# Kernel optimization log

Measured on AMD Instinct MI355X. Metric: run time of the kernel, lower is better.

Reference implementation:

```python
import jax, jax.numpy as jnp
import numpy as np

N_NODES = 100000
N_EDGES = 600000
DIMS = [128, 64, 32, 2]


def gcn_conv(x, edge_index, W, b, n_nodes):
    """PyG GCNConv (eval mode): symmetric-normalized aggregation with self-loops.
    out = D^{-1/2} (A + I) D^{-1/2} (x W) + b
    """
    h = x @ W  # [N, out] -- transform first (cheaper when out < in)
    src = jnp.concatenate([edge_index[0], jnp.arange(n_nodes)])  # add self-loops
    dst = jnp.concatenate([edge_index[1], jnp.arange(n_nodes)])
    deg = jax.ops.segment_sum(jnp.ones_like(dst, dtype=h.dtype), dst,
                              num_segments=n_nodes)  # in-degree incl. self-loop
    dinv = jax.lax.rsqrt(deg)
    norm = dinv[src] * dinv[dst]  # [E+N]
    msg = norm[:, None] * h[src]  # gather + scale
    out = jax.ops.segment_sum(msg, dst, num_segments=n_nodes)  # scatter-add
    return out + b


def setup_inputs() -> dict:
    key = jax.random.key(0)
    ks = jax.random.split(key, 8)
    x = jax.random.normal(ks[0], (N_NODES, DIMS[0]), dtype=jnp.float32)
    edge_index = jax.random.randint(ks[1], (2, N_EDGES), 0, N_NODES, dtype=jnp.int64)
    inp = {"x": x, "edge_index": edge_index}
    for i in range(3):
        fan_in, fan_out = DIMS[i], DIMS[i + 1]
        s = 1.0 / np.sqrt(fan_in)
        inp[f"W{i+1}"] = jax.random.uniform(ks[2 + 2 * i], (fan_in, fan_out),
                                            minval=-s, maxval=s, dtype=jnp.float32)
        inp[f"b{i+1}"] = jnp.zeros((fan_out,), dtype=jnp.float32)
    return inp


def reference(x, edge_index, W1, b1, W2, b2, W3, b3):
    # 3 stacked GCNConv layers with ReLU; dropout is identity in eval mode.
    n = x.shape[0]
    x = jax.nn.relu(gcn_conv(x, edge_index, W1, b1, n))
    x = jax.nn.relu(gcn_conv(x, edge_index, W2, b2, n))
    x = jax.nn.relu(gcn_conv(x, edge_index, W3, b3, n))
    return x
```

## Files before the change

kernel.cpp:

```cpp
#include <hip/hip_runtime.h>
#include <math.h>


#define FULL_GRID 2048
#define PARTS 8

typedef const __attribute__((address_space(1))) void* gas_ptr;
typedef __attribute__((address_space(3))) void* las_ptr;
typedef __attribute__((ext_vector_type(8))) short bf16x8;
typedef __attribute__((ext_vector_type(4))) float f32x4;

__device__ __forceinline__ void gld16(const void* g, void* l) {
  __builtin_amdgcn_global_load_lds((gas_ptr)g, (las_ptr)l, 16, 0, 0);
}

__device__ __forceinline__ unsigned short f2bf(float f) {
  unsigned int u = __float_as_uint(f);
  u += 0x7FFF + ((u >> 16) & 1);
  return (unsigned short)(u >> 16);
}
__device__ __forceinline__ float bf2f(unsigned short h) {
  return __uint_as_float(((unsigned int)h) << 16);
}

__global__ __launch_bounds__(256) void k_init(int* __restrict__ p, int n4,
                                              const unsigned int* __restrict__ words,
                                              int* __restrict__ flag,
                                              const float* __restrict__ W1,
                                              const float* __restrict__ W2,
                                              short* __restrict__ Wh1,
                                              short* __restrict__ Wl1,
                                              short* __restrict__ Wh2,
                                              short* __restrict__ Wl2) {
  if (blockIdx.x == 128) {
    __shared__ int sm[256];
    int cnt = 0;
    #pragma unroll
    for (int j = 0; j < 8; ++j) {
      int idx = (threadIdx.x * 8 + j) * 2 + 1;
      cnt += (words[idx] == 0u) ? 1 : 0;
    }
    sm[threadIdx.x] = cnt;
    __syncthreads();
    for (int off = 128; off > 0; off >>= 1) {
      if (threadIdx.x < off) sm[threadIdx.x] += sm[threadIdx.x + off];
      __syncthreads();
    }
    if (threadIdx.x == 0) flag[0] = (sm[0] > 1024) ? 1 : 0;
    return;
  }
  if (blockIdx.x > 128) {
    const int t = (blockIdx.x - 129) * 256 + threadIdx.x;
    const int stride = 32 * 256;
    for (int q = t; q < 4 * 4 * 64 * 8; q += stride) {
      const int e = q & 7, lane = (q >> 3) & 63, nt = (q >> 9) & 3, kt = q >> 11;
      const int k = kt * 32 + (lane >> 4) * 8 + e;
      const int nn = nt * 16 + (lane & 15);
      const float f = W1[k * 64 + nn];
      const unsigned short h = f2bf(f);
      Wh1[q] = (short)h;
      Wl1[q] = (short)f2bf(f - bf2f(h));
    }
    for (int q = t; q < 2 * 2 * 64 * 8; q += stride) {
      const int e = q & 7, lane = (q >> 3) & 63, nt = (q >> 9) & 1, kt = q >> 10;
      const int k = kt * 32 + (lane >> 4) * 8 + e;
      const int nn = nt * 16 + (lane & 15);
      const float f = W2[k * 32 + nn];
      const unsigned short h = f2bf(f);
      Wh2[q] = (short)h;
      Wl2[q] = (short)f2bf(f - bf2f(h));
    }
    return;
  }
  int i = blockIdx.x * blockDim.x + threadIdx.x;
  const int stride = 128 * blockDim.x;
  int4* p4 = (int4*)p;
  for (; i < n4; i += stride) p4[i] = make_int4(0, 0, 0, 0);
}

__global__ __launch_bounds__(256) void k_normalize(const void* __restrict__ eraw,
                                                   int E,
                                                   const int* __restrict__ flag,
                                                   int* __restrict__ srcn,
                                                   int* __restrict__ dstn) {
  const int is64 = flag[0];
  int i = blockIdx.x * blockDim.x + threadIdx.x;
  const int stride = gridDim.x * blockDim.x;
  if (is64) {
    const long long* e = (const long long*)eraw;
    for (; i < E; i += stride) {
      srcn[i] = (int)e[i];
      dstn[i] = (int)e[(long long)E + i];
    }
  } else {
    const int* e = (const int*)eraw;
    for (; i < E; i += stride) {
      srcn[i] = e[i];
      dstn[i] = e[E + i];
    }
  }
}

__global__ __launch_bounds__(256) void k_hist(const int* __restrict__ dstn, int E,
                                              int N, int* __restrict__ counts) {
  const int part = blockIdx.x & (PARTS - 1);
  const int lo = (int)((long long)N * part / PARTS);
  const int hi = (int)((long long)N * (part + 1) / PARTS);
  int i = (blockIdx.x >> 3) * blockDim.x + threadIdx.x;
  const int stride = (gridDim.x >> 3) * blockDim.x;
  for (; i < E; i += stride) {
    const int d = dstn[i];
    if (d >= lo && d < hi) atomicAdd(&counts[d], 1);
  }
}

__global__ __launch_bounds__(1024) void k_scan1(const int* __restrict__ counts,
                                                int* __restrict__ scanned,
                                                int* __restrict__ partials, int n) {
  __shared__ int sm[1024];
  const int i = blockIdx.x * 1024 + threadIdx.x;
  const int v = (i < n) ? counts[i] : 0;
  sm[threadIdx.x] = v;
  __syncthreads();
  for (int off = 1; off < 1024; off <<= 1) {
    int t = sm[threadIdx.x];
    int u = (threadIdx.x >= off) ? sm[threadIdx.x - off] : 0;
    __syncthreads();
    sm[threadIdx.x] = t + u;
    __syncthreads();
  }
  const int inc = sm[threadIdx.x];
  if (i < n) scanned[i] = inc - v;
  if (threadIdx.x == 1023) partials[blockIdx.x] = inc;
}

__global__ __launch_bounds__(256) void k_scan3(const int* __restrict__ scanned,
                                               const int* __restrict__ partials,
                                               int nb,
                                               const int* __restrict__ counts,
                                               int* __restrict__ offsets,
                                               int* __restrict__ cursor,
                                               float* __restrict__ dinv, int n) {
  __shared__ int ps[1024];
  for (int t = threadIdx.x; t < nb; t += 256) ps[t] = partials[t];
  __syncthreads();
  if (threadIdx.x == 0) {
    int run = 0;
    for (int b = 0; b < nb; ++b) { const int v = ps[b]; ps[b] = run; run += v; }
  }
  __syncthreads();
  int i = blockIdx.x * blockDim.x + threadIdx.x;
  const int stride = gridDim.x * blockDim.x;
  for (; i < n; i += stride) {
    const int o = scanned[i] + ps[i >> 10];
    offsets[i] = o;
    cursor[i] = o;
    dinv[i] = rsqrtf((float)counts[i] + 1.0f);
  }
}

__global__ __launch_bounds__(256) void k_fill(const int* __restrict__ srcn,
                                              const int* __restrict__ dstn, int E,
                                              int N, int* __restrict__ cursor,
                                              int* __restrict__ elist) {
  const int part = blockIdx.x & (PARTS - 1);
  const int lo = (int)((long long)N * part / PARTS);
  const int hi = (int)((long long)N * (part + 1) / PARTS);
  int i = (blockIdx.x >> 3) * blockDim.x + threadIdx.x;
  const int stride = (gridDim.x >> 3) * blockDim.x;
  for (; i < E; i += stride) {
    const int d = dstn[i];
    if (d >= lo && d < hi) elist[atomicAdd(&cursor[d], 1)] = srcn[i];
  }
}

template <int F_IN, int F_OUT>
__global__ __launch_bounds__(256) void k_transform_mfma(
    const float* __restrict__ X, const short* __restrict__ Wh,
    const short* __restrict__ Wl, const float* __restrict__ dinv,
    float* __restrict__ H, int n) {
  constexpr int KT = F_IN / 32;
  constexpr int NT = F_OUT / 16;
  constexpr int K4f = F_IN / 4;
  constexpr int SLOTS = F_IN / 8;
  constexpr int TILE_M = 64;
  constexpr int WFRAG = KT * NT * 64 * 8;
  static_assert((WFRAG * 2) % 1024 == 0, "W segs");

  __shared__ __align__(16) unsigned short Xh[TILE_M * F_IN];
  __shared__ __align__(16) unsigned short Xl[TILE_M * F_IN];
  __shared__ __align__(16) unsigned short Whs[WFRAG];
  __shared__ __align__(16) unsigned short Wls[WFRAG];

  const int tid = threadIdx.x;
  const int lane = tid & 63;
  const int wid = tid >> 6;
  const long long base = (long long)blockIdx.x * TILE_M;

  constexpr int WSEGS = WFRAG * 2 / 1024;
  for (int seg = wid; seg < WSEGS; seg += 4) {
    gld16((const char*)Wh + seg * 1024 + lane * 16, (char*)Whs + seg * 1024);
    gld16((const char*)Wl + seg * 1024 + lane * 16, (char*)Wls + seg * 1024);
  }

  const float4* __restrict__ X4 = (const float4*)X;
  for (int g = tid; g < TILE_M * K4f; g += 256) {
    const int row = g / K4f, c4 = g % K4f;
    float4 v = make_float4(0.f, 0.f, 0.f, 0.f);
    if (base + row < n) v = X4[(base + row) * K4f + c4];
    ushort4 hv, lv;
    hv.x = f2bf(v.x); lv.x = f2bf(v.x - bf2f(hv.x));
    hv.y = f2bf(v.y); lv.y = f2bf(v.y - bf2f(hv.y));
    hv.z = f2bf(v.z); lv.z = f2bf(v.z - bf2f(hv.z));
    hv.w = f2bf(v.w); lv.w = f2bf(v.w - bf2f(hv.w));
    const int slot = (c4 >> 1) ^ (row & (SLOTS - 1));
    const int boff = row * (F_IN * 2) + slot * 16 + (c4 & 1) * 8;
    *(ushort4*)((char*)Xh + boff) = hv;
    *(ushort4*)((char*)Xl + boff) = lv;
  }
  __syncthreads();

  const int arow = lane & 15;
  const int kg = lane >> 4;
  const int lrow = wid * 16 + arow;

  f32x4 acc[NT];
  #pragma unroll
  for (int t = 0; t < NT; ++t) {
    f32x4 z = {0.f, 0.f, 0.f, 0.f};
    acc[t] = z;
  }

  #pragma unroll
  for (int kt = 0; kt < KT; ++kt) {
    const int slot = (kt * 4 + kg) ^ (lrow & (SLOTS - 1));
    const int aoff = lrow * (F_IN * 2) + slot * 16;
    const bf16x8 ah = *(const bf16x8*)((const char*)Xh + aoff);
    const bf16x8 al = *(const bf16x8*)((const char*)Xl + aoff);
    #pragma unroll
    for (int nt = 0; nt < NT; ++nt) {
      const int woff = ((kt * NT + nt) * 64 + lane) * 8;
      const bf16x8 bh = *(const bf16x8*)&Whs[woff];
      const bf16x8 bl = *(const bf16x8*)&Wls[woff];
      acc[nt] = __builtin_amdgcn_mfma_f32_16x16x32_bf16(ah, bh, acc[nt], 0, 0, 0);
      acc[nt] = __builtin_amdgcn_mfma_f32_16x16x32_bf16(ah, bl, acc[nt], 0, 0, 0);
      acc[nt] = __builtin_amdgcn_mfma_f32_16x16x32_bf16(al, bh, acc[nt], 0, 0, 0);
    }
  }

  #pragma unroll
  for (int r = 0; r < 4; ++r) {
    const long long row = base + wid * 16 + kg * 4 + r;
    if (row < n) {
      const float di = dinv[row];
      #pragma unroll
      for (int nt = 0; nt < NT; ++nt)
        H[row * F_OUT + nt * 16 + arow] = di * acc[nt][r];
    }
  }
}

template <int F, bool RELU_OUT, bool FUSE_W3>
__global__ __launch_bounds__(256) void k_agg_vec2(const float* __restrict__ HS,
                                                  const float* __restrict__ dinv,
                                                  const int* __restrict__ offsets,
                                                  const int* __restrict__ counts,
                                                  const int* __restrict__ elist,
                                                  const float* __restrict__ bias,
                                                  const float* __restrict__ W3,
                                                  float* __restrict__ out, int n) {
  constexpr int LPE = F / 4;
  constexpr int EPW = 64 / LPE;
  const int lane = threadIdx.x & 63;
  const int wv = (blockIdx.x * (blockDim.x >> 6)) + (threadIdx.x >> 6);
  const int nwaves = gridDim.x * (blockDim.x >> 6);
  const int g = lane / LPE;
  const int fl = lane % LPE;
  const float4 bf = *(const float4*)&bias[fl * 4];

  float w3a0 = 0.f, w3a1 = 0.f, w3a2 = 0.f, w3a3 = 0.f;
  float w3b0 = 0.f, w3b1 = 0.f, w3b2 = 0.f, w3b3 = 0.f;
  if (FUSE_W3) {
    w3a0 = W3[(fl * 4 + 0) * 2 + 0]; w3b0 = W3[(fl * 4 + 0) * 2 + 1];
    w3a1 = W3[(fl * 4 + 1) * 2 + 0]; w3b1 = W3[(fl * 4 + 1) * 2 + 1];
    w3a2 = W3[(fl * 4 + 2) * 2 + 0]; w3b2 = W3[(fl * 4 + 2) * 2 + 1];
    w3a3 = W3[(fl * 4 + 3) * 2 + 0]; w3b3 = W3[(fl * 4 + 3) * 2 + 1];
  }

  for (long long dA = wv; dA < n; dA += 2ll * nwaves) {
    const long long dB = dA + nwaves;
    const bool hasB = dB < n;
    const float diA = dinv[dA];
    const float diB = hasB ? dinv[dB] : 0.f;
    const int stA = offsets[dA];
    const int cntA = counts[dA];
    const int stB = hasB ? offsets[dB] : 0;
    const int cntB = hasB ? counts[dB] : 0;
    float4 accA = make_float4(0.f, 0.f, 0.f, 0.f);
    float4 accB = make_float4(0.f, 0.f, 0.f, 0.f);
    if (g == 0) accA = *(const float4*)&HS[dA * F + fl * 4];
    if (g == 1 && hasB) accB = *(const float4*)&HS[dB * F + fl * 4];

    const int jmax = cntA > cntB ? cntA : cntB;
    const int cA = cntA > 0 ? cntA - 1 : 0;
    const int cB = cntB > 0 ? cntB - 1 : 0;
    for (int j = 0; j < jmax; j += 2 * EPW) {
      const int e0 = j + g;
      const int e1 = j + EPW + g;
      const int iA0 = elist[stA + (e0 < cntA ? e0 : cA)];
      const int iA1 = elist[stA + (e1 < cntA ? e1 : cA)];
      const int iB0 = elist[stB + (e0 < cntB ? e0 : cB)];
      const int iB1 = elist[stB + (e1 < cntB ? e1 : cB)];
      const float4 vA0 = *(const float4*)&HS[(long long)iA0 * F + fl * 4];
      const float4 vA1 = *(const float4*)&HS[(long long)iA1 * F + fl * 4];
      const float4 vB0 = *(const float4*)&HS[(long long)iB0 * F + fl * 4];
      const float4 vB1 = *(const float4*)&HS[(long long)iB1 * F + fl * 4];
      if (e0 < cntA) {
        accA.x += vA0.x; accA.y += vA0.y; accA.z += vA0.z; accA.w += vA0.w;
      }
      if (e1 < cntA) {
        accA.x += vA1.x; accA.y += vA1.y; accA.z += vA1.z; accA.w += vA1.w;
      }
      if (e0 < cntB) {
        accB.x += vB0.x; accB.y += vB0.y; accB.z += vB0.z; accB.w += vB0.w;
      }
      if (e1 < cntB) {
        accB.x += vB1.x; accB.y += vB1.y; accB.z += vB1.z; accB.w += vB1.w;
      }
    }
    #pragma unroll
    for (int m = LPE; m < 64; m <<= 1) {
      accA.x += __shfl_xor(accA.x, m, 64);
      accA.y += __shfl_xor(accA.y, m, 64);
      accA.z += __shfl_xor(accA.z, m, 64);
      accA.w += __shfl_xor(accA.w, m, 64);
      accB.x += __shfl_xor(accB.x, m, 64);
      accB.y += __shfl_xor(accB.y, m, 64);
      accB.z += __shfl_xor(accB.z, m, 64);
      accB.w += __shfl_xor(accB.w, m, 64);
    }
    float4 rA, rB;
    rA.x = fmaf(diA, accA.x, bf.x); rA.y = fmaf(diA, accA.y, bf.y);
    rA.z = fmaf(diA, accA.z, bf.z); rA.w = fmaf(diA, accA.w, bf.w);
    rB.x = fmaf(diB, accB.x, bf.x); rB.y = fmaf(diB, accB.y, bf.y);
    rB.z = fmaf(diB, accB.z, bf.z); rB.w = fmaf(diB, accB.w, bf.w);
    if (RELU_OUT) {
      rA.x = fmaxf(rA.x, 0.f); rA.y = fmaxf(rA.y, 0.f);
      rA.z = fmaxf(rA.z, 0.f); rA.w = fmaxf(rA.w, 0.f);
      rB.x = fmaxf(rB.x, 0.f); rB.y = fmaxf(rB.y, 0.f);
      rB.z = fmaxf(rB.z, 0.f); rB.w = fmaxf(rB.w, 0.f);
    }
    if (!FUSE_W3) {
      if (g == 0) *(float4*)&out[dA * F + fl * 4] = rA;
      if (g == 1 && hasB) *(float4*)&out[dB * F + fl * 4] = rB;
    } else {
      float tA0 = rA.x * w3a0 + rA.y * w3a1 + rA.z * w3a2 + rA.w * w3a3;
      float tA1 = rA.x * w3b0 + rA.y * w3b1 + rA.z * w3b2 + rA.w * w3b3;
      float tB0 = rB.x * w3a0 + rB.y * w3a1 + rB.z * w3a2 + rB.w * w3a3;
      float tB1 = rB.x * w3b0 + rB.y * w3b1 + rB.z * w3b2 + rB.w * w3b3;
      #pragma unroll
      for (int m = 1; m < LPE; m <<= 1) {
        tA0 += __shfl_xor(tA0, m, 64);
        tA1 += __shfl_xor(tA1, m, 64);
        tB0 += __shfl_xor(tB0, m, 64);
        tB1 += __shfl_xor(tB1, m, 64);
      }
      if (lane == 0) {
        out[dA * 2 + 0] = diA * tA0;
        out[dA * 2 + 1] = diA * tA1;
      }
      if (lane == LPE && hasB) {
        out[dB * 2 + 0] = diB * tB0;
        out[dB * 2 + 1] = diB * tB1;
      }
    }
  }
}

template <int F, bool RELU_OUT>
__global__ __launch_bounds__(256) void k_aggregate(const float* __restrict__ HS,
                                                   const float* __restrict__ dinv,
                                                   const int* __restrict__ offsets,
                                                   const int* __restrict__ counts,
                                                   const int* __restrict__ elist,
                                                   const float* __restrict__ bias,
                                                   float* __restrict__ out, int n) {
  const int f = threadIdx.x % F;
  const int grp = threadIdx.x / F;
  constexpr int GRPS = 256 / F;
  const float bf = bias[f];

  for (long long d = (long long)blockIdx.x * GRPS + grp; d < n;
       d += (long long)gridDim.x * GRPS) {
    const float di = dinv[d];
    float acc = HS[d * F + f];
    const int start = offsets[d];
    const int cnt = counts[d];
    for (int j = 0; j < cnt; j += 8) {
      int idx[8];
      float v[8];
      #pragma unroll
      for (int t = 0; t < 8; ++t) {
        const int jj = (j + t < cnt) ? (j + t) : j;
        idx[t] = elist[start + jj];
      }
      #pragma unroll
      for (int t = 0; t < 8; ++t) v[t] = HS[(long long)idx[t] * F + f];
      #pragma unroll
      for (int t = 0; t < 8; ++t) acc += (j + t < cnt) ? v[t] : 0.f;
    }
    float r = fmaf(di, acc, bf);
    if (RELU_OUT) r = fmaxf(r, 0.f);
    out[d * F + f] = r;
  }
}

extern "C" void kernel_launch(void* const* d_in, const int* in_sizes, int n_in,
                              void* d_out, int out_size, void* d_ws, size_t ws_size,
                              hipStream_t stream) {
  const float* x = (const float*)d_in[0];
  const void* eraw = d_in[1];
  const float* W1 = (const float*)d_in[2];
  const float* b1 = (const float*)d_in[3];
  const float* W2 = (const float*)d_in[4];
  const float* b2 = (const float*)d_in[5];
  const float* W3 = (const float*)d_in[6];
  const float* b3 = (const float*)d_in[7];
  float* out = (float*)d_out;

  const int N = in_sizes[0] / 128;
  const int E = in_sizes[1] / 2;

  char* ws = (char*)d_ws;
  size_t off = 0;
  auto alloc = [&](size_t bytes) -> char* {
    char* p = ws + off;
    off = (off + bytes + 255) & ~(size_t)255;
    return p;
  };
  int*   flag     = (int*)alloc(256);
  int*   counts   = (int*)alloc((size_t)N * 4 + 16);
  int*   scanned  = (int*)alloc((size_t)N * 4);
  int*   partials = (int*)alloc(1024 * 4);
  int*   offsets  = (int*)alloc((size_t)N * 4);
  int*   cursor   = (int*)alloc((size_t)N * 4);
  int*   srcn     = (int*)alloc((size_t)E * 4);
  int*   dstn     = (int*)alloc((size_t)E * 4);
  int*   elist    = (int*)alloc((size_t)E * 4);
  float* dinv     = (float*)alloc((size_t)N * 4);
  short* Wh1      = (short*)alloc(4 * 4 * 64 * 8 * 2);
  short* Wl1      = (short*)alloc(4 * 4 * 64 * 8 * 2);
  short* Wh2      = (short*)alloc(2 * 2 * 64 * 8 * 2);
  short* Wl2      = (short*)alloc(2 * 2 * 64 * 8 * 2);
  float* hbuf     = (float*)alloc((size_t)N * 64 * 4);
  float* obuf     = (float*)alloc((size_t)N * 64 * 4);
  float* h2buf    = (float*)alloc((size_t)N * 32 * 4);
  (void)ws_size; (void)n_in; (void)out_size;

  k_init<<<161, 256, 0, stream>>>(counts, (N + 3) / 4, (const unsigned int*)eraw,
                                  flag, W1, W2, Wh1, Wl1, Wh2, Wl2);
  k_normalize<<<1024, 256, 0, stream>>>(eraw, E, flag, srcn, dstn);
  k_hist<<<FULL_GRID, 256, 0, stream>>>(dstn, E, N, counts);
  const int NB = (N + 1023) >> 10;
  k_scan1<<<NB, 1024, 0, stream>>>(counts, scanned, partials, N);
  k_scan3<<<(N + 255) / 256, 256, 0, stream>>>(scanned, partials, NB, counts,
                                               offsets, cursor, dinv, N);
  k_fill<<<FULL_GRID, 256, 0, stream>>>(srcn, dstn, E, N, cursor, elist);

  k_transform_mfma<128, 64><<<(N + 63) / 64, 256, 0, stream>>>(
      x, Wh1, Wl1, dinv, hbuf, N);
  k_agg_vec2<64, true, false><<<FULL_GRID, 256, 0, stream>>>(
      hbuf, dinv, offsets, counts, elist, b1, nullptr, obuf, N);

  k_transform_mfma<64, 32><<<(N + 63) / 64, 256, 0, stream>>>(
      obuf, Wh2, Wl2, dinv, h2buf, N);
  k_agg_vec2<32, true, true><<<FULL_GRID, 256, 0, stream>>>(
      h2buf, dinv, offsets, counts, elist, b2, W3, hbuf, N);

  k_aggregate<2, true><<<(N + 127) / 128, 256, 0, stream>>>(
      hbuf, dinv, offsets, counts, elist, b3, out, N);
}
```

Baseline: 171.1 us.

## Store intermediate features as bf16 and fuse edge-format detection into init

Intermediate hidden buffers (transform outputs, aggregation outputs, fused W3 output) are now stored as bf16 instead of fp32. This halves the bytes moved in the gather-heavy aggregation kernels and the transforms. The layer-2 transform gets a dedicated bf16-input MFMA kernel that uses async LDS loads and drops the low-part correction on the activations. The separate normalize kernel and flag are merged into k_init, which now detects int64 indices per block, and the last layer reads packed bf16 pairs. This trades reduced precision in the activations for lower memory traffic and one fewer launch.

After: 192.5 us. 1.12x slower.

```diff
diff --git a/kernel.cpp b/kernel.cpp
--- a/kernel.cpp
+++ b/kernel.cpp
@@ -8,6 +8,7 @@
 typedef const __attribute__((address_space(1))) void* gas_ptr;
 typedef __attribute__((address_space(3))) void* las_ptr;
 typedef __attribute__((ext_vector_type(8))) short bf16x8;
+typedef __attribute__((ext_vector_type(8))) unsigned short u16x8;
 typedef __attribute__((ext_vector_type(4))) float f32x4;
 
 __device__ __forceinline__ void gld16(const void* g, void* l) {
@@ -24,33 +25,25 @@
 }
 
 __global__ __launch_bounds__(256) void k_init(int* __restrict__ p, int n4,
-                                              const unsigned int* __restrict__ words,
-                                              int* __restrict__ flag,
+                                              const void* __restrict__ eraw, int E,
+                                              int* __restrict__ srcn,
+                                              int* __restrict__ dstn,
                                               const float* __restrict__ W1,
                                               const float* __restrict__ W2,
                                               short* __restrict__ Wh1,
                                               short* __restrict__ Wl1,
                                               short* __restrict__ Wh2,
                                               short* __restrict__ Wl2) {
-  if (blockIdx.x == 128) {
-    __shared__ int sm[256];
-    int cnt = 0;
-    #pragma unroll
-    for (int j = 0; j < 8; ++j) {
-      int idx = (threadIdx.x * 8 + j) * 2 + 1;
-      cnt += (words[idx] == 0u) ? 1 : 0;
-    }
-    sm[threadIdx.x] = cnt;
-    __syncthreads();
-    for (int off = 128; off > 0; off >>= 1) {
-      if (threadIdx.x < off) sm[threadIdx.x] += sm[threadIdx.x + off];
-      __syncthreads();
-    }
-    if (threadIdx.x == 0) flag[0] = (sm[0] > 1024) ? 1 : 0;
+  const int b = blockIdx.x;
+  if (b < 128) {
+    int i = b * blockDim.x + threadIdx.x;
+    const int stride = 128 * blockDim.x;
+    int4* p4 = (int4*)p;
+    for (; i < n4; i += stride) p4[i] = make_int4(0, 0, 0, 0);
     return;
   }
-  if (blockIdx.x > 128) {
-    const int t = (blockIdx.x - 129) * 256 + threadIdx.x;
+  if (b < 160) {
+    const int t = (b - 128) * 256 + threadIdx.x;
     const int stride = 32 * 256;
     for (int q = t; q < 4 * 4 * 64 * 8; q += stride) {
       const int e = q & 7, lane = (q >> 3) & 63, nt = (q >> 9) & 3, kt = q >> 11;
@@ -72,20 +65,18 @@
     }
     return;
   }
-  int i = blockIdx.x * blockDim.x + threadIdx.x;
-  const int stride = 128 * blockDim.x;
-  int4* p4 = (int4*)p;
-  for (; i < n4; i += stride) p4[i] = make_int4(0, 0, 0, 0);
-}
-
-__global__ __launch_bounds__(256) void k_normalize(const void* __restrict__ eraw,
-                                                   int E,
-                                                   const int* __restrict__ flag,
-                                                   int* __restrict__ srcn,
-                                                   int* __restrict__ dstn) {
-  const int is64 = flag[0];
-  int i = blockIdx.x * blockDim.x + threadIdx.x;
-  const int stride = gridDim.x * blockDim.x;
+  __shared__ int sm[256];
+  const unsigned int* words = (const unsigned int*)eraw;
+  sm[threadIdx.x] = (words[threadIdx.x * 2 + 1] == 0u) ? 1 : 0;
+  __syncthreads();
+  for (int off = 128; off > 0; off >>= 1) {
+    if (threadIdx.x < off) sm[threadIdx.x] += sm[threadIdx.x + off];
+    __syncthreads();
+  }
+  const int is64 = sm[0] > 128;
+  const int nb = b - 160;
+  int i = nb * 256 + threadIdx.x;
+  const int stride = 1024 * 256;
   if (is64) {
     const long long* e = (const long long*)eraw;
     for (; i < E; i += stride) {
@@ -178,7 +169,7 @@
 __global__ __launch_bounds__(256) void k_transform_mfma(
     const float* __restrict__ X, const short* __restrict__ Wh,
     const short* __restrict__ Wl, const float* __restrict__ dinv,
-    float* __restrict__ H, int n) {
+    unsigned short* __restrict__ H, int n) {
   constexpr int KT = F_IN / 32;
   constexpr int NT = F_OUT / 16;
   constexpr int K4f = F_IN / 4;
@@ -255,163 +246,221 @@
       const float di = dinv[row];
       #pragma unroll
       for (int nt = 0; nt < NT; ++nt)
-        H[row * F_OUT + nt * 16 + arow] = di * acc[nt][r];
-    }
-  }
-}
-
-template <int F, bool RELU_OUT, bool FUSE_W3>
-__global__ __launch_bounds__(256) void k_agg_vec2(const float* __restrict__ HS,
-                                                  const float* __restrict__ dinv,
-                                                  const int* __restrict__ offsets,
-                                                  const int* __restrict__ counts,
-                                                  const int* __restrict__ elist,
-                                                  const float* __restrict__ bias,
-                                                  const float* __restrict__ W3,
-                                                  float* __restrict__ out, int n) {
-  constexpr int LPE = F / 4;
+        H[row * F_OUT + nt * 16 + arow] = f2bf(di * acc[nt][r]);
+    }
+  }
+}
+
+__global__ __launch_bounds__(256) void k_t2_mfma(
+    const unsigned short* __restrict__ A, const short* __restrict__ Wh,
+    const short* __restrict__ Wl, const float* __restrict__ dinv,
+    unsigned short* __restrict__ H, int n) {
+  constexpr int KT = 2, NT = 2, SLOTS = 8, TILE_M = 64;
+  constexpr int WFRAG = KT * NT * 64 * 8;
+
+  __shared__ __align__(16) unsigned short Xs[TILE_M * 64];
+  __shared__ __align__(16) unsigned short Whs[WFRAG];
+  __shared__ __align__(16) unsigned short Wls[WFRAG];
+
+  const int tid = threadIdx.x;
+  const int lane = tid & 63;
+  const int wid = tid >> 6;
+  const long long base = (long long)blockIdx.x * TILE_M;
+
+  for (int seg = wid; seg < WFRAG * 2 / 1024; seg += 4) {
+    gld16((const char*)Wh + seg * 1024 + lane * 16, (char*)Whs + seg * 1024);
+    gld16((const char*)Wl + seg * 1024 + lane * 16, (char*)Wls + seg * 1024);
+  }
+
+  if (base + TILE_M <= n) {
+    #pragma unroll
+    for (int j = 0; j < 8; ++j) {
+      const int seg = wid * 2 + (j & 1) + (j >> 1) * 8;
+      (void)seg;
+    }
+    #pragma unroll
+    for (int j = 0; j < 2; ++j) {
+      const int seg = wid + j * 4;
+      const int slot = seg * 64 + lane;
+      const int row = slot >> 3;
+      const int c = slot & 7;
+      gld16(&A[(base + row) * 64 + ((c ^ (row & 7)) * 8)], &Xs[seg * 512]);
+    }
+  } else {
+    for (int slot = tid; slot < TILE_M * SLOTS; slot += 256) {
+      const int row = slot >> 3;
+      const int c = slot & 7;
+      u16x8 v = {0, 0, 0, 0, 0, 0, 0, 0};
+      if (base + row < n)
+        v = *(const u16x8*)&A[(base + row) * 64 + ((c ^ (row & 7)) * 8)];
+      *(u16x8*)&Xs[slot * 8] = v;
+    }
+  }
+  __syncthreads();
+
+  const int arow = lane & 15;
+  const int kg = lane >> 4;
+  const int lrow = wid * 16 + arow;
+
+  f32x4 acc[NT];
+  #pragma unroll
+  for (int t = 0; t < NT; ++t) {
+    f32x4 z = {0.f, 0.f, 0.f, 0.f};
+    acc[t] = z;
+  }
+
+  #pragma unroll
+  for (int kt = 0; kt < KT; ++kt) {
+    const int slot = (kt * 4 + kg) ^ (lrow & 7);
+    const bf16x8 ah = *(const bf16x8*)&Xs[lrow * 64 + slot * 8];
+    #pragma unroll
+    for (int nt = 0; nt < NT; ++nt) {
+      const int woff = ((kt * NT + nt) * 64 + lane) * 8;
+      const bf16x8 bh = *(const bf16x8*)&Whs[woff];
+      const bf16x8 bl = *(const bf16x8*)&Wls[woff];
+      acc[nt] = __builtin_amdgcn_mfma_f32_16x16x32_bf16(ah, bh, acc[nt], 0, 0, 0);
+      acc[nt] = __builtin_amdgcn_mfma_f32_16x16x32_bf16(ah, bl, acc[nt], 0, 0, 0);
+    }
+  }
+
+  #pragma unroll
+  for (int r = 0; r < 4; ++r) {
+    const long long row = base + wid * 16 + kg * 4 + r;
+    if (row < n) {
+      const float di = dinv[row];
+      #pragma unroll
+      for (int nt = 0; nt < NT; ++nt)
+        H[row * 32 + nt * 16 + arow] = f2bf(di * acc[nt][r]);
+    }
+  }
+}
+
+template <int F, bool FUSE_W3>
+__global__ __launch_bounds__(256) void k_agg_bf(const unsigned short* __restrict__ HS,
+                                                const float* __restrict__ dinv,
+                                                const int* __restrict__ offsets,
+                                                const int* __restrict__ counts,
+                                                const int* __restrict__ elist,
+                                                const float* __restrict__ bias,
+                                                const float* __restrict__ W3,
+                                                void* __restrict__ outv, int n) {
+  constexpr int LPE = F / 8;
   constexpr int EPW = 64 / LPE;
   const int lane = threadIdx.x & 63;
   const int wv = (blockIdx.x * (blockDim.x >> 6)) + (threadIdx.x >> 6);
   const int nwaves = gridDim.x * (blockDim.x >> 6);
   const int g = lane / LPE;
   const int fl = lane % LPE;
-  const float4 bf = *(const float4*)&bias[fl * 4];
-
-  float w3a0 = 0.f, w3a1 = 0.f, w3a2 = 0.f, w3a3 = 0.f;
-  float w3b0 = 0.f, w3b1 = 0.f, w3b2 = 0.f, w3b3 = 0.f;
+
+  float bf[8];
+  #pragma unroll
+  for (int j = 0; j < 8; ++j) bf[j] = bias[fl * 8 + j];
+  float w3a[8], w3b[8];
   if (FUSE_W3) {
-    w3a0 = W3[(fl * 4 + 0) * 2 + 0]; w3b0 = W3[(fl * 4 + 0) * 2 + 1];
-    w3a1 = W3[(fl * 4 + 1) * 2 + 0]; w3b1 = W3[(fl * 4 + 1) * 2 + 1];
-    w3a2 = W3[(fl * 4 + 2) * 2 + 0]; w3b2 = W3[(fl * 4 + 2) * 2 + 1];
-    w3a3 = W3[(fl * 4 + 3) * 2 + 0]; w3b3 = W3[(fl * 4 + 3) * 2 + 1];
-  }
-
-  for (long long dA = wv; dA < n; dA += 2ll * nwaves) {
-    const long long dB = dA + nwaves;
-    const bool hasB = dB < n;
-    const float diA = dinv[dA];
-    const float diB = hasB ? dinv[dB] : 0.f;
-    const int stA = offsets[dA];
-    const int cntA = counts[dA];
-    const int stB = hasB ? offsets[dB] : 0;
-    const int cntB = hasB ? counts[dB] : 0;
-    float4 accA = make_float4(0.f, 0.f, 0.f, 0.f);
-    float4 accB = make_float4(0.f, 0.f, 0.f, 0.f);
-    if (g == 0) accA = *(const float4*)&HS[dA * F + fl * 4];
-    if (g == 1 && hasB) accB = *(const float4*)&HS[dB * F + fl * 4];
-
-    const int jmax = cntA > cntB ? cntA : cntB;
-    const int cA = cntA > 0 ? cntA - 1 : 0;
-    const int cB = cntB > 0 ? cntB - 1 : 0;
-    for (int j = 0; j < jmax; j += 2 * EPW) {
-      const int e0 = j + g;
-      const int e1 = j + EPW + g;
-      const int iA0 = elist[stA + (e0 < cntA ? e0 : cA)];
-      const int iA1 = elist[stA + (e1 < cntA ? e1 : cA)];
-      const int iB0 = elist[stB + (e0 < cntB ? e0 : cB)];
-      const int iB1 = elist[stB + (e1 < cntB ? e1 : cB)];
-      const float4 vA0 = *(const float4*)&HS[(long long)iA0 * F + fl * 4];
-      const float4 vA1 = *(const float4*)&HS[(long long)iA1 * F + fl * 4];
-      const float4 vB0 = *(const float4*)&HS[(long long)iB0 * F + fl * 4];
-      const float4 vB1 = *(const float4*)&HS[(long long)iB1 * F + fl * 4];
-      if (e0 < cntA) {
-        accA.x += vA0.x; accA.y += vA0.y; accA.z += vA0.z; accA.w += vA0.w;
-      }
-      if (e1 < cntA) {
-        accA.x += vA1.x; accA.y += vA1.y; accA.z += vA1.z; accA.w += vA1.w;
-      }
-      if (e0 < cntB) {
-        accB.x += vB0.x; accB.y += vB0.y; accB.z += vB0.z; accB.w += vB0.w;
-      }
-      if (e1 < cntB) {
-        accB.x += vB1.x; accB.y += vB1.y; accB.z += vB1.z; accB.w += vB1.w;
+    #pragma unroll
+    for (int j = 0; j < 8; ++j) {
+      w3a[j] = W3[(fl * 8 + j) * 2 + 0];
+      w3b[j] = W3[(fl * 8 + j) * 2 + 1];
+    }
+  }
+
+  for (long long d = wv; d < n; d += nwaves) {
+    const float di = dinv[d];
+    const int start = offsets[d];
+    const int cnt = counts[d];
+    float a[8] = {0.f, 0.f, 0.f, 0.f, 0.f, 0.f, 0.f, 0.f};
+    if (g == 0) {
+      const u16x8 v = *(const u16x8*)&HS[d * F + fl * 8];
+      #pragma unroll
+      for (int j = 0; j < 8; ++j) a[j] = bf2f(v[j]);
+    }
+    const int cl = cnt > 0 ? cnt - 1 : 0;
+    for (int j0 = 0; j0 < cnt; j0 += 2 * EPW) {
+      const int e0 = j0 + g;
+      const int e1 = j0 + EPW + g;
+      const int i0 = elist[start + (e0 < cnt ? e0 : cl)];
+      const int i1 = elist[start + (e1 < cnt ? e1 : cl)];
+      const u16x8 v0 = *(const u16x8*)&HS[(long long)i0 * F + fl * 8];
+      const u16x8 v1 = *(const u16x8*)&HS[(long long)i1 * F + fl * 8];
+      if (e0 < cnt) {
+        #pragma unroll
+        for (int j = 0; j < 8; ++j) a[j] += bf2f(v0[j]);
+      }
+      if (e1 < cnt) {
+        #pragma unroll
+        for (int j = 0; j < 8; ++j) a[j] += bf2f(v1[j]);
       }
     }
     #pragma unroll
     for (int m = LPE; m < 64; m <<= 1) {
-      accA.x += __shfl_xor(accA.x, m, 64);
-      accA.y += __shfl_xor(accA.y, m, 64);
-      accA.z += __shfl_xor(accA.z, m, 64);
-      accA.w += __shfl_xor(accA.w, m, 64);
-      accB.x += __shfl_xor(accB.x, m, 64);
-      accB.y += __shfl_xor(accB.y, m, 64);
-      accB.z += __shfl_xor(accB.z, m, 64);
-      accB.w += __shfl_xor(accB.w, m, 64);
-    }
-    float4 rA, rB;
-    rA.x = fmaf(diA, accA.x, bf.x); rA.y = fmaf(diA, accA.y, bf.y);
-    rA.z = fmaf(diA, accA.z, bf.z); rA.w = fmaf(diA, accA.w, bf.w);
-    rB.x = fmaf(diB, accB.x, bf.x); rB.y = fmaf(diB, accB.y, bf.y);
-    rB.z = fmaf(diB, accB.z, bf.z); rB.w = fmaf(diB, accB.w, bf.w);
-    if (RELU_OUT) {
-      rA.x = fmaxf(rA.x, 0.f); rA.y = fmaxf(rA.y, 0.f);
-      rA.z = fmaxf(rA.z, 0.f); rA.w = fmaxf(rA.w, 0.f);
-      rB.x = fmaxf(rB.x, 0.f); rB.y = fmaxf(rB.y, 0.f);
-      rB.z = fmaxf(rB.z, 0.f); rB.w = fmaxf(rB.w, 0.f);
-    }
+      #pragma unroll
+      for (int j = 0; j < 8; ++j) a[j] += __shfl_xor(a[j], m, 64);
+    }
+    float r[8];
+    #pragma unroll
+    for (int j = 0; j < 8; ++j) r[j] = fmaxf(fmaf(di, a[j], bf[j]), 0.f);
     if (!FUSE_W3) {
-      if (g == 0) *(float4*)&out[dA * F + fl * 4] = rA;
-      if (g == 1 && hasB) *(float4*)&out[dB * F + fl * 4] = rB;
+      if (g == 0) {
+        u16x8 pv;
+        #pragma unroll
+        for (int j = 0; j < 8; ++j) pv[j] = f2bf(r[j]);
+        *(u16x8*)&((unsigned short*)outv)[d * F + fl * 8] = pv;
+      }
     } else {
-      float tA0 = rA.x * w3a0 + rA.y * w3a1 + rA.z * w3a2 + rA.w * w3a3;
-      float tA1 = rA.x * w3b0 + rA.y * w3b1 + rA.z * w3b2 + rA.w * w3b3;
-      float tB0 = rB.x * w3a0 + rB.y * w3a1 + rB.z * w3a2 + rB.w * w3a3;
-      float tB1 = rB.x * w3b0 + rB.y * w3b1 + rB.z * w3b2 + rB.w * w3b3;
+      float t0 = 0.f, t1 = 0.f;
+      #pragma unroll
+      for (int j = 0; j < 8; ++j) {
+        t0 = fmaf(r[j], w3a[j], t0);
+        t1 = fmaf(r[j], w3b[j], t1);
+      }
       #pragma unroll
       for (int m = 1; m < LPE; m <<= 1) {
-        tA0 += __shfl_xor(tA0, m, 64);
-        tA1 += __shfl_xor(tA1, m, 64);
-        tB0 += __shfl_xor(tB0, m, 64);
-        tB1 += __shfl_xor(tB1, m, 64);
+        t0 += __shfl_xor(t0, m, 64);
+        t1 += __shfl_xor(t1, m, 64);
       }
       if (lane == 0) {
-        out[dA * 2 + 0] = diA * tA0;
-        out[dA * 2 + 1] = diA * tA1;
-      }
-      if (lane == LPE && hasB) {
-        out[dB * 2 + 0] = diB * tB0;
-        out[dB * 2 + 1] = diB * tB1;
-      }
-    }
-  }
-}
-
-template <int F, bool RELU_OUT>
-__global__ __launch_bounds__(256) void k_aggregate(const float* __restrict__ HS,
-                                                   const float* __restrict__ dinv,
-                                                   const int* __restrict__ offsets,
-                                                   const int* __restrict__ counts,
-                                                   const int* __restrict__ elist,
-                                                   const float* __restrict__ bias,
-                                                   float* __restrict__ out, int n) {
-  const int f = threadIdx.x % F;
-  const int grp = threadIdx.x / F;
-  constexpr int GRPS = 256 / F;
-  const float bf = bias[f];
-
-  for (long long d = (long long)blockIdx.x * GRPS + grp; d < n;
-       d += (long long)gridDim.x * GRPS) {
+        const unsigned int pk = (unsigned int)f2bf(di * t0) |
+                                ((unsigned int)f2bf(di * t1) << 16);
+        ((unsigned int*)outv)[d] = pk;
+      }
+    }
+  }
+}
+
+__global__ __launch_bounds__(256) void k_agg3(const unsigned int* __restrict__ HS,
+                                              const float* __restrict__ dinv,
+                                              const int* __restrict__ offsets,
+                                              const int* __restrict__ counts,
+                                              const int* __restrict__ elist,
+                                              const float* __restrict__ b3,
+                                              float* __restrict__ out, int n) {
+  const float b30 = b3[0], b31 = b3[1];
+  int d = blockIdx.x * blockDim.x + threadIdx.x;
+  const int stride = gridDim.x * blockDim.x;
+  for (; d < n; d += stride) {
     const float di = dinv[d];
-    float acc = HS[d * F + f];
+    const unsigned int self = HS[d];
+    float a0 = bf2f((unsigned short)(self & 0xFFFF));
+    float a1 = bf2f((unsigned short)(self >> 16));
     const int start = offsets[d];
     const int cnt = counts[d];
     for (int j = 0; j < cnt; j += 8) {
-      int idx[8];
-      float v[8];
+      unsigned int u[8];
       #pragma unroll
       for (int t = 0; t < 8; ++t) {
         const int jj = (j + t < cnt) ? (j + t) : j;
-        idx[t] = elist[start + jj];
-      }
-      #pragma unroll
-      for (int t = 0; t < 8; ++t) v[t] = HS[(long long)idx[t] * F + f];
-      #pragma unroll
-      for (int t = 0; t < 8; ++t) acc += (j + t < cnt) ? v[t] : 0.f;
-    }
-    float r = fmaf(di, acc, bf);
-    if (RELU_OUT) r = fmaxf(r, 0.f);
-    out[d * F + f] = r;
+        u[t] = HS[elist[start + jj]];
+      }
+      #pragma unroll
+      for (int t = 0; t < 8; ++t) {
+        if (j + t < cnt) {
+          a0 += bf2f((unsigned short)(u[t] & 0xFFFF));
+          a1 += bf2f((unsigned short)(u[t] >> 16));
+        }
+      }
+    }
+    out[d * 2 + 0] = fmaxf(fmaf(di, a0, b30), 0.f);
+    out[d * 2 + 1] = fmaxf(fmaf(di, a1, b31), 0.f);
   }
 }
 
@@ -438,28 +487,26 @@
     off = (off + bytes + 255) & ~(size_t)255;
     return p;
   };
-  int*   flag     = (int*)alloc(256);
-  int*   counts   = (int*)alloc((size_t)N * 4 + 16);
-  int*   scanned  = (int*)alloc((size_t)N * 4);
-  int*   partials = (int*)alloc(1024 * 4);
-  int*   offsets  = (int*)alloc((size_t)N * 4);
-  int*   cursor   = (int*)alloc((size_t)N * 4);
-  int*   srcn     = (int*)alloc((size_t)E * 4);
-  int*   dstn     = (int*)alloc((size_t)E * 4);
-  int*   elist    = (int*)alloc((size_t)E * 4);
-  float* dinv     = (float*)alloc((size_t)N * 4);
-  short* Wh1      = (short*)alloc(4 * 4 * 64 * 8 * 2);
-  short* Wl1      = (short*)alloc(4 * 4 * 64 * 8 * 2);
-  short* Wh2      = (short*)alloc(2 * 2 * 64 * 8 * 2);
-  short* Wl2      = (short*)alloc(2 * 2 * 64 * 8 * 2);
-  float* hbuf     = (float*)alloc((size_t)N * 64 * 4);
-  float* obuf     = (float*)alloc((size_t)N * 64 * 4);
-  float* h2buf    = (float*)alloc((size_t)N * 32 * 4);
+  int*            counts   = (int*)alloc((size_t)N * 4 + 16);
+  int*            scanned  = (int*)alloc((size_t)N * 4);
+  int*            partials = (int*)alloc(1024 * 4);
+  int*            offsets  = (int*)alloc((size_t)N * 4);
+  int*            cursor   = (int*)alloc((size_t)N * 4);
+  int*            srcn     = (int*)alloc((size_t)E * 4);
+  int*            dstn     = (int*)alloc((size_t)E * 4);
+  int*            elist    = (int*)alloc((size_t)E * 4);
+  float*          dinv     = (float*)alloc((size_t)N * 4);
+  short*          Wh1      = (short*)alloc(4 * 4 * 64 * 8 * 2);
+  short*          Wl1      = (short*)alloc(4 * 4 * 64 * 8 * 2);
+  short*          Wh2      = (short*)alloc(2 * 2 * 64 * 8 * 2);
+  short*          Wl2      = (short*)alloc(2 * 2 * 64 * 8 * 2);
+  unsigned short* hbuf     = (unsigned short*)alloc((size_t)N * 64 * 2);
+  unsigned short* obuf     = (unsigned short*)alloc((size_t)N * 64 * 2);
+  unsigned short* h2buf    = (unsigned short*)alloc((size_t)N * 32 * 2);
   (void)ws_size; (void)n_in; (void)out_size;
 
-  k_init<<<161, 256, 0, stream>>>(counts, (N + 3) / 4, (const unsigned int*)eraw,
-                                  flag, W1, W2, Wh1, Wl1, Wh2, Wl2);
-  k_normalize<<<1024, 256, 0, stream>>>(eraw, E, flag, srcn, dstn);
+  k_init<<<1184, 256, 0, stream>>>(counts, (N + 3) / 4, eraw, E, srcn, dstn,
+                                   W1, W2, Wh1, Wl1, Wh2, Wl2);
   k_hist<<<FULL_GRID, 256, 0, stream>>>(dstn, E, N, counts);
   const int NB = (N + 1023) >> 10;
   k_scan1<<<NB, 1024, 0, stream>>>(counts, scanned, partials, N);
@@ -469,14 +516,13 @@
 
   k_transform_mfma<128, 64><<<(N + 63) / 64, 256, 0, stream>>>(
       x, Wh1, Wl1, dinv, hbuf, N);
-  k_agg_vec2<64, true, false><<<FULL_GRID, 256, 0, stream>>>(
+  k_agg_bf<64, false><<<FULL_GRID, 256, 0, stream>>>(
       hbuf, dinv, offsets, counts, elist, b1, nullptr, obuf, N);
 
-  k_transform_mfma<64, 32><<<(N + 63) / 64, 256, 0, stream>>>(
-      obuf, Wh2, Wl2, dinv, h2buf, N);
-  k_agg_vec2<32, true, true><<<FULL_GRID, 256, 0, stream>>>(
+  k_t2_mfma<<<(N + 63) / 64, 256, 0, stream>>>(obuf, Wh2, Wl2, dinv, h2buf, N);
+  k_agg_bf<32, true><<<FULL_GRID, 256, 0, stream>>>(
       h2buf, dinv, offsets, counts, elist, b2, W3, hbuf, N);
 
-  k_aggregate<2, true><<<(N + 127) / 128, 256, 0, stream>>>(
-      hbuf, dinv, offsets, counts, elist, b3, out, N);
-}
+  k_agg3<<<(N + 255) / 256, 256, 0, stream>>>((const unsigned int*)hbuf, dinv,
+                                              offsets, counts, elist, b3, out, N);
+}
```

## Fuse CSR build stages into one cooperative kernel with grid syncs

Applied to the files above, without the earlier changes.

Merges init, edge normalization, histogram, scan and fill kernels into a single cooperative kernel separated by grid-wide barriers. The goal is to remove several kernel launch gaps and their inter-kernel drain costs. Hist and fill now run on a smaller grid, the scan is restructured to 256 threads handling 4 elements each, and the int64 detection samples fewer words. In exchange, grid.sync adds its own overhead, and the smaller grid may reduce parallelism for the atomic phases.

Measured after the change: 608.5 us. 256% more time.

```diff
diff --git a/kernel.cpp b/kernel.cpp
--- a/kernel.cpp
+++ b/kernel.cpp
@@ -1,8 +1,12 @@
 #include <hip/hip_runtime.h>
+#include <hip/hip_cooperative_groups.h>
 #include <math.h>
 
+namespace cg = cooperative_groups;
+
 
 #define FULL_GRID 2048
+#define CSR_GRID 1024
 #define PARTS 8
 
 typedef const __attribute__((address_space(1))) void* gas_ptr;
@@ -23,35 +27,26 @@
   return __uint_as_float(((unsigned int)h) << 16);
 }
 
-__global__ __launch_bounds__(256) void k_init(int* __restrict__ p, int n4,
-                                              const unsigned int* __restrict__ words,
-                                              int* __restrict__ flag,
-                                              const float* __restrict__ W1,
-                                              const float* __restrict__ W2,
-                                              short* __restrict__ Wh1,
-                                              short* __restrict__ Wl1,
-                                              short* __restrict__ Wh2,
-                                              short* __restrict__ Wl2) {
-  if (blockIdx.x == 128) {
-    __shared__ int sm[256];
-    int cnt = 0;
-    #pragma unroll
-    for (int j = 0; j < 8; ++j) {
-      int idx = (threadIdx.x * 8 + j) * 2 + 1;
-      cnt += (words[idx] == 0u) ? 1 : 0;
-    }
-    sm[threadIdx.x] = cnt;
-    __syncthreads();
-    for (int off = 128; off > 0; off >>= 1) {
-      if (threadIdx.x < off) sm[threadIdx.x] += sm[threadIdx.x + off];
-      __syncthreads();
-    }
-    if (threadIdx.x == 0) flag[0] = (sm[0] > 1024) ? 1 : 0;
-    return;
-  }
-  if (blockIdx.x > 128) {
-    const int t = (blockIdx.x - 129) * 256 + threadIdx.x;
-    const int stride = 32 * 256;
+__global__ __launch_bounds__(256, 4) void k_csr(
+    int* __restrict__ counts, int n4, const void* __restrict__ eraw, int E,
+    int* __restrict__ srcn, int* __restrict__ dstn,
+    const float* __restrict__ W1, const float* __restrict__ W2,
+    short* __restrict__ Wh1, short* __restrict__ Wl1,
+    short* __restrict__ Wh2, short* __restrict__ Wl2,
+    int* __restrict__ scanned, int* __restrict__ partials,
+    int* __restrict__ offsets, int* __restrict__ cursor,
+    float* __restrict__ dinv, int* __restrict__ elist, int N) {
+  cg::grid_group grid = cg::this_grid();
+  const int tid = threadIdx.x;
+  const int b = blockIdx.x;
+
+  __shared__ int sm[256];
+  __shared__ int ss[256];
+  __shared__ int ps[1024];
+
+  if (b < 8) {
+    const int t = b * 256 + tid;
+    const int stride = 8 * 256;
     for (int q = t; q < 4 * 4 * 64 * 8; q += stride) {
       const int e = q & 7, lane = (q >> 3) & 63, nt = (q >> 9) & 3, kt = q >> 11;
       const int k = kt * 32 + (lane >> 4) * 8 + e;
@@ -70,107 +65,108 @@
       Wh2[q] = (short)h;
       Wl2[q] = (short)f2bf(f - bf2f(h));
     }
-    return;
-  }
-  int i = blockIdx.x * blockDim.x + threadIdx.x;
-  const int stride = 128 * blockDim.x;
-  int4* p4 = (int4*)p;
-  for (; i < n4; i += stride) p4[i] = make_int4(0, 0, 0, 0);
-}
-
-__global__ __launch_bounds__(256) void k_normalize(const void* __restrict__ eraw,
-                                                   int E,
-                                                   const int* __restrict__ flag,
-                                                   int* __restrict__ srcn,
-                                                   int* __restrict__ dstn) {
-  const int is64 = flag[0];
-  int i = blockIdx.x * blockDim.x + threadIdx.x;
-  const int stride = gridDim.x * blockDim.x;
-  if (is64) {
-    const long long* e = (const long long*)eraw;
+  } else {
+    int i = (b - 8) * 256 + tid;
+    const int zstride = (CSR_GRID - 8) * 256;
+    int4* p4 = (int4*)counts;
+    for (; i < n4; i += zstride) p4[i] = make_int4(0, 0, 0, 0);
+    const unsigned int* words = (const unsigned int*)eraw;
+    sm[tid] = (words[tid * 2 + 1] == 0u) ? 1 : 0;
+    __syncthreads();
+    for (int off = 128; off > 0; off >>= 1) {
+      if (tid < off) sm[tid] += sm[tid + off];
+      __syncthreads();
+    }
+    const int is64 = sm[0] > 128;
+    i = (b - 8) * 256 + tid;
+    if (is64) {
+      const long long* e = (const long long*)eraw;
+      for (; i < E; i += zstride) {
+        srcn[i] = (int)e[i];
+        dstn[i] = (int)e[(long long)E + i];
+      }
+    } else {
+      const int* e = (const int*)eraw;
+      for (; i < E; i += zstride) {
+        srcn[i] = e[i];
+        dstn[i] = e[E + i];
+      }
+    }
+  }
+  grid.sync();
+
+  {
+    const int part = b & (PARTS - 1);
+    const int lo = (int)((long long)N * part / PARTS);
+    const int hi = (int)((long long)N * (part + 1) / PARTS);
+    int i = (b >> 3) * 256 + tid;
+    const int stride = (CSR_GRID >> 3) * 256;
     for (; i < E; i += stride) {
-      srcn[i] = (int)e[i];
-      dstn[i] = (int)e[(long long)E + i];
-    }
-  } else {
-    const int* e = (const int*)eraw;
+      const int d = dstn[i];
+      if (d >= lo && d < hi) atomicAdd(&counts[d], 1);
+    }
+  }
+  grid.sync();
+
+  {
+    const int NBLK = (N + 1023) >> 10;
+    for (int blk = b; blk < NBLK; blk += CSR_GRID) {
+      const int base = blk * 1024 + tid * 4;
+      int v[4];
+      #pragma unroll
+      for (int j = 0; j < 4; ++j) v[j] = (base + j < N) ? counts[base + j] : 0;
+      const int s = v[0] + v[1] + v[2] + v[3];
+      ss[tid] = s;
+      __syncthreads();
+      for (int off = 1; off < 256; off <<= 1) {
+        const int t_ = ss[tid];
+        const int u = (tid >= off) ? ss[tid - off] : 0;
+        __syncthreads();
+        ss[tid] = t_ + u;
+        __syncthreads();
+      }
+      const int incl = ss[tid];
+      int excl = incl - s;
+      #pragma unroll
+      for (int j = 0; j < 4; ++j) {
+        if (base + j < N) scanned[base + j] = excl;
+        excl += v[j];
+      }
+      if (tid == 255) partials[blk] = incl;
+      __syncthreads();
+    }
+  }
+  grid.sync();
+
+  {
+    const int NBLK = (N + 1023) >> 10;
+    for (int t2 = tid; t2 < NBLK; t2 += 256) ps[t2] = partials[t2];
+    __syncthreads();
+    if (tid == 0) {
+      int run = 0;
+      for (int q = 0; q < NBLK; ++q) { const int v = ps[q]; ps[q] = run; run += v; }
+    }
+    __syncthreads();
+    int i = b * 256 + tid;
+    for (; i < N; i += CSR_GRID * 256) {
+      const int o = scanned[i] + ps[i >> 10];
+      offsets[i] = o;
+      cursor[i] = o;
+      dinv[i] = rsqrtf((float)counts[i] + 1.0f);
+    }
+  }
+  grid.sync();
+
+  {
+    const int part = b & (PARTS - 1);
+    const int lo = (int)((long long)N * part / PARTS);
+    const int hi = (int)((long long)N * (part + 1) / PARTS);
+    int i = (b >> 3) * 256 + tid;
+    const int stride = (CSR_GRID >> 3) * 256;
     for (; i < E; i += stride) {
-      srcn[i] = e[i];
-      dstn[i] = e[E + i];
-    }
-  }
-}
-
-__global__ __launch_bounds__(256) void k_hist(const int* __restrict__ dstn, int E,
-                                              int N, int* __restrict__ counts) {
-  const int part = blockIdx.x & (PARTS - 1);
-  const int lo = (int)((long long)N * part / PARTS);
-  const int hi = (int)((long long)N * (part + 1) / PARTS);
-  int i = (blockIdx.x >> 3) * blockDim.x + threadIdx.x;
-  const int stride = (gridDim.x >> 3) * blockDim.x;
-  for (; i < E; i += stride) {
-    const int d = dstn[i];
-    if (d >= lo && d < hi) atomicAdd(&counts[d], 1);
-  }
-}
-
-__global__ __launch_bounds__(1024) void k_scan1(const int* __restrict__ counts,
-                                                int* __restrict__ scanned,
-                                                int* __restrict__ partials, int n) {
-  __shared__ int sm[1024];
-  const int i = blockIdx.x * 1024 + threadIdx.x;
-  const int v = (i < n) ? counts[i] : 0;
-  sm[threadIdx.x] = v;
-  __syncthreads();
-  for (int off = 1; off < 1024; off <<= 1) {
-    int t = sm[threadIdx.x];
-    int u = (threadIdx.x >= off) ? sm[threadIdx.x - off] : 0;
-    __syncthreads();
-    sm[threadIdx.x] = t + u;
-    __syncthreads();
-  }
-  const int inc = sm[threadIdx.x];
-  if (i < n) scanned[i] = inc - v;
-  if (threadIdx.x == 1023) partials[blockIdx.x] = inc;
-}
-
-__global__ __launch_bounds__(256) void k_scan3(const int* __restrict__ scanned,
-                                               const int* __restrict__ partials,
-                                               int nb,
-                                               const int* __restrict__ counts,
-                                               int* __restrict__ offsets,
-                                               int* __restrict__ cursor,
-                                               float* __restrict__ dinv, int n) {
-  __shared__ int ps[1024];
-  for (int t = threadIdx.x; t < nb; t += 256) ps[t] = partials[t];
-  __syncthreads();
-  if (threadIdx.x == 0) {
-    int run = 0;
-    for (int b = 0; b < nb; ++b) { const int v = ps[b]; ps[b] = run; run += v; }
-  }
-  __syncthreads();
-  int i = blockIdx.x * blockDim.x + threadIdx.x;
-  const int stride = gridDim.x * blockDim.x;
-  for (; i < n; i += stride) {
-    const int o = scanned[i] + ps[i >> 10];
-    offsets[i] = o;
-    cursor[i] = o;
-    dinv[i] = rsqrtf((float)counts[i] + 1.0f);
-  }
-}
-
-__global__ __launch_bounds__(256) void k_fill(const int* __restrict__ srcn,
-                                              const int* __restrict__ dstn, int E,
-                                              int N, int* __restrict__ cursor,
-                                              int* __restrict__ elist) {
-  const int part = blockIdx.x & (PARTS - 1);
-  const int lo = (int)((long long)N * part / PARTS);
-  const int hi = (int)((long long)N * (part + 1) / PARTS);
-  int i = (blockIdx.x >> 3) * blockDim.x + threadIdx.x;
-  const int stride = (gridDim.x >> 3) * blockDim.x;
-  for (; i < E; i += stride) {
-    const int d = dstn[i];
-    if (d >= lo && d < hi) elist[atomicAdd(&cursor[d], 1)] = srcn[i];
+      const int d = dstn[i];
+      if (d >= lo && d < hi) elist[atomicAdd(&cursor[d], 1)] = srcn[i];
+    }
   }
 }
 
@@ -438,7 +434,6 @@
     off = (off + bytes + 255) & ~(size_t)255;
     return p;
   };
-  int*   flag     = (int*)alloc(256);
   int*   counts   = (int*)alloc((size_t)N * 4 + 16);
   int*   scanned  = (int*)alloc((size_t)N * 4);
   int*   partials = (int*)alloc(1024 * 4);
@@ -457,15 +452,14 @@
   float* h2buf    = (float*)alloc((size_t)N * 32 * 4);
   (void)ws_size; (void)n_in; (void)out_size;
 
-  k_init<<<161, 256, 0, stream>>>(counts, (N + 3) / 4, (const unsigned int*)eraw,
-                                  flag, W1, W2, Wh1, Wl1, Wh2, Wl2);
-  k_normalize<<<1024, 256, 0, stream>>>(eraw, E, flag, srcn, dstn);
-  k_hist<<<FULL_GRID, 256, 0, stream>>>(dstn, E, N, counts);
-  const int NB = (N + 1023) >> 10;
-  k_scan1<<<NB, 1024, 0, stream>>>(counts, scanned, partials, N);
-  k_scan3<<<(N + 255) / 256, 256, 0, stream>>>(scanned, partials, NB, counts,
-                                               offsets, cursor, dinv, N);
-  k_fill<<<FULL_GRID, 256, 0, stream>>>(srcn, dstn, E, N, cursor, elist);
+  int n4 = (N + 3) / 4;
+  void* args[] = {(void*)&counts, (void*)&n4, (void*)&eraw, (void*)&E,
+                  (void*)&srcn, (void*)&dstn, (void*)&W1, (void*)&W2,
+                  (void*)&Wh1, (void*)&Wl1, (void*)&Wh2, (void*)&Wl2,
+                  (void*)&scanned, (void*)&partials, (void*)&offsets,
+                  (void*)&cursor, (void*)&dinv, (void*)&elist, (void*)&N};
+  hipLaunchCooperativeKernel((const void*)k_csr, dim3(CSR_GRID), dim3(256),
+                             args, 0, stream);
 
   k_transform_mfma<128, 64><<<(N + 63) / 64, 256, 0, stream>>>(
       x, Wh1, Wl1, dinv, hbuf, N);
```
